# Performance work log

Hardware: AMD Instinct MI355X
Metric: run time of the kernel (lower is better)

## Reference

```python
import jax, jax.numpy as jnp
import numpy as np

B, S, D = 8, 2048, 512

def setup_inputs() -> dict:
    key = jax.random.key(0)
    k1, k2 = jax.random.split(key)
    x = jax.random.normal(k1, (B, S, D), dtype=jnp.float32)
    # nn.Parameter(torch.rand(D, D)) -> uniform [0, 1)
    attn_matrix = jax.random.uniform(k2, (D, D), dtype=jnp.float32)
    return {"x": x, "attn_matrix": attn_matrix}

def reference(x, attn_matrix):
    # scalar = sqrt(last dim of x)
    scale = jnp.sqrt(jnp.asarray(x.shape[-1], dtype=x.dtype))
    # prod = x @ W @ x^T / sqrt(D)  -> [B, S, S]
    xw = jnp.einsum('bsd,de->bse', x, attn_matrix)
    prod = jnp.einsum('bse,bte->bst', xw, x) / scale
    scores = jax.nn.softmax(prod, axis=-1)
    out = jnp.einsum('bst,btd->bsd', scores, x)
    return out
```

## Files before the change

kernel.cpp:

```cpp
#include <hip/hip_runtime.h>
#include <math.h>

#define B_ 8
#define S_ 2048
#define D_ 512
#define HSZ (B_ * S_ * D_)

typedef _Float16 half8 __attribute__((ext_vector_type(8)));
typedef _Float16 half4h __attribute__((ext_vector_type(4)));
typedef __fp16 fp16x2 __attribute__((ext_vector_type(2)));
typedef float f32x4 __attribute__((ext_vector_type(4)));
typedef float f32x16 __attribute__((ext_vector_type(16)));
typedef unsigned int u32;
typedef u32 u32x4 __attribute__((ext_vector_type(4)));

constexpr float INV_SCALE = 0.044194173824159216f;

__device__ __forceinline__ u32 pk16(float a, float b) {
    fp16x2 r = __builtin_amdgcn_cvt_pkrtz(a, b);
    union { fp16x2 h; u32 u; } U; U.h = r; return U.u;
}

__device__ __forceinline__ int offK(int t, int d) {
    return ((t >> 5) << 14) | (((d >> 7) & 3) << 12) | (((d >> 4) & 7) << 9) |
           ((t & 31) << 4) | (((d >> 3) & 1) << 3) | (d & 7);
}
__device__ __forceinline__ int offV(int t, int d) {
    return ((t >> 5) << 14) | (((d >> 7) & 3) << 12) | (((d >> 5) & 3) << 10) |
           (((t >> 4) & 1) << 9) | ((d & 31) << 4) | (((t >> 3) & 1) << 3) | (t & 7);
}
__device__ __forceinline__ int offWT(int n, int k) {
    return ((n >> 5) << 14) | ((k >> 4) << 9) | ((n & 31) << 4) |
           (((k >> 3) & 1) << 3) | (k & 7);
}

__global__ __launch_bounds__(256) void cvt_all(const float* __restrict__ x,
                                               const float* __restrict__ W,
                                               _Float16* __restrict__ xK,
                                               _Float16* __restrict__ xV,
                                               _Float16* __restrict__ WT) {
    __shared__ float T[64 * 65];
    const int tid = threadIdx.x;
    const int blk = blockIdx.x;

    const float* src;
    int t0, d0, isX, bofs = 0;
    if (blk < 2048) {
        int b = blk >> 8;
        int r = blk & 255;
        t0 = (r >> 3) * 64; d0 = (r & 7) * 64;
        src = x + (size_t)b * (S_ * D_);
        bofs = b * (S_ * D_);
        isX = 1;
    } else {
        int r = blk - 2048;
        t0 = (r >> 3) * 64; d0 = (r & 7) * 64;
        src = W;
        isX = 0;
    }

#pragma unroll
    for (int it = 0; it < 4; ++it) {
        int flat = it * 256 + tid;
        int row = flat >> 4, c4 = (flat & 15) * 4;
        float4 v = *(const float4*)(src + (size_t)(t0 + row) * 512 + d0 + c4);
        T[row * 65 + c4 + 0] = v.x; T[row * 65 + c4 + 1] = v.y;
        T[row * 65 + c4 + 2] = v.z; T[row * 65 + c4 + 3] = v.w;
        if (isX) {
            half4h h = { (_Float16)v.x, (_Float16)v.y, (_Float16)v.z, (_Float16)v.w };
            *(half4h*)(xK + bofs + offK(t0 + row, d0 + c4)) = h;
        }
    }
    __syncthreads();
#pragma unroll
    for (int it = 0; it < 2; ++it) {
        int flat = it * 256 + tid;
        int d = flat >> 3, c = (flat & 7) * 8;
        half8 hv;
#pragma unroll
        for (int j = 0; j < 8; ++j) hv[j] = (_Float16)T[(c + j) * 65 + d];
        if (isX)
            *(half8*)(xV + bofs + offV(t0 + c, d0 + d)) = hv;
        else
            *(half8*)(WT + offWT(d0 + d, t0 + c)) = hv;
    }
}

__global__ __launch_bounds__(256, 2) void gemm8(const _Float16* __restrict__ xK,
                                                const _Float16* __restrict__ WT,
                                                _Float16* __restrict__ qwh) {
    const int tid = threadIdx.x;
    const int w = tid >> 6, lane = tid & 63;
    const int r31 = lane & 31, hi = lane >> 5;
    const int laneoff = (r31 << 4) + (hi << 3);
    const int blk = blockIdx.x;
    const int nb = blk & 3;
    const int mb = blk >> 2;
    const int n0w = nb * 128 + w * 32;
    const int batch = mb >> 4;
    const int mt0 = (mb & 15) * 4;
    const size_t bb = (size_t)batch * (S_ * D_);

    half8 Bf[32];
    const _Float16* wb = WT + ((n0w >> 5) << 14) + laneoff;
#pragma unroll
    for (int kc = 0; kc < 32; ++kc) Bf[kc] = *(const half8*)(wb + (kc << 9));

    const _Float16* ab = xK + bb + laneoff;
    const int kk = n0w + r31;
    const int qterm = (((kk >> 7) & 3) << 12) + (((kk >> 4) & 7) << 9) +
                      (((kk >> 3) & 1) << 3) + (kk & 7);

#pragma unroll
    for (int mt = 0; mt < 4; ++mt) {
        const _Float16* at = ab + ((mt0 + mt) << 14);
        f32x16 ca, cb;
#pragma unroll
        for (int r = 0; r < 16; ++r) { ca[r] = 0.f; cb[r] = 0.f; }
#pragma unroll
        for (int kg = 0; kg < 4; ++kg) {
            half8 Af[8];
#pragma unroll
            for (int k8 = 0; k8 < 8; ++k8)
                Af[k8] = *(const half8*)(at + ((kg * 8 + k8) << 9));
#pragma unroll
            for (int k8 = 0; k8 < 8; k8 += 2) {
                ca = __builtin_amdgcn_mfma_f32_32x32x16_f16(Af[k8],     Bf[kg * 8 + k8],     ca, 0, 0, 0);
                cb = __builtin_amdgcn_mfma_f32_32x32x16_f16(Af[k8 + 1], Bf[kg * 8 + k8 + 1], cb, 0, 0, 0);
            }
        }
        _Float16* qp = qwh + bb + ((mt0 + mt) << 14) + qterm;
#pragma unroll
        for (int r = 0; r < 16; ++r) {
            int mrow = (r & 3) + ((r >> 2) << 3) + (hi << 2);
            qp[mrow << 4] = (_Float16)((ca[r] + cb[r]) * INV_SCALE);
        }
    }
}

__global__ __launch_bounds__(256, 2)
void flashP(const _Float16* __restrict__ xK, const _Float16* __restrict__ xV,
            const _Float16* __restrict__ qwh, float* __restrict__ out) {
    __shared__ __align__(16) unsigned char SMEM[34816];
    float* Sx = (float*)SMEM;

    const int tid = threadIdx.x;
    const int w = tid >> 6, lane = tid & 63;
    const int r31 = lane & 31, hi = lane >> 5;
    const int laneoff = (r31 << 4) + (hi << 3);
    const int d0w = w * 128;
    const int bx = blockIdx.x;
    const int b = bx & 7;
    const int q0 = (bx >> 3) * 32;
    const size_t xb = (size_t)b * (S_ * D_);

    half8 Qr[8];
    {
        const _Float16* qb = qwh + xb + ((q0 >> 5) << 14) + (w << 12) + laneoff;
#pragma unroll
        for (int kc = 0; kc < 8; ++kc)
            Qr[kc] = *(const half8*)(qb + (kc << 9));
    }

    const _Float16* kbase = xK + xb + (w << 12) + laneoff;
    const _Float16* vbase = xV + xb + (w << 12) + laneoff;

    half8 KA[8], KB[8];
    f32x16 sS;

#pragma unroll
    for (int kc = 0; kc < 8; ++kc)
        KA[kc] = *(const half8*)(kbase + (kc << 9));
    {
        f32x16 s;
#pragma unroll
        for (int r = 0; r < 16; ++r) s[r] = 0.f;
#pragma unroll
        for (int kc = 0; kc < 8; ++kc)
            s = __builtin_amdgcn_mfma_f32_32x32x16_f16(KA[kc], Qr[kc], s, 0, 0, 0);
        sS = s;
    }
#pragma unroll
    for (int kc = 0; kc < 8; ++kc)
        KB[kc] = *(const half8*)(kbase + (1 << 14) + (kc << 9));
    {
        float* sxw = Sx + w * 1024;
#pragma unroll
        for (int r2 = 0; r2 < 4; ++r2) {
            f32x4 v_ = { sS[4 * r2 + 0], sS[4 * r2 + 1], sS[4 * r2 + 2], sS[4 * r2 + 3] };
            *(f32x4*)&sxw[(r2 * 64 + lane) * 4] = v_;
        }
    }
    __syncthreads();

    f32x16 O[4];
#pragma unroll
    for (int dc = 0; dc < 4; ++dc)
#pragma unroll
        for (int r = 0; r < 16; ++r) O[dc][r] = 0.f;
    float m = -1e30f, l = 0.f;

#define SMX_HEAD(TI) \
    half8 Vc[8]; \
    _Pragma("unroll") for (int dc = 0; dc < 4; ++dc) \
    _Pragma("unroll") for (int kh = 0; kh < 2; ++kh) \
        Vc[dc * 2 + kh] = *(const half8*)(vbase + ((TI) << 14) + (dc << 10) + (kh << 9)); \
    float sv[16]; \
    { \
        _Pragma("unroll") for (int i = 0; i < 16; ++i) sv[i] = sS[i]; \
        _Pragma("unroll") for (int pw = 1; pw < 4; ++pw) { \
            const float* sxp = Sx + (((TI) & 1) * 4 + (w ^ pw)) * 1024; \
            _Pragma("unroll") for (int r2 = 0; r2 < 4; ++r2) { \
                f32x4 pp = *(const f32x4*)&sxp[(r2 * 64 + lane) * 4]; \
                _Pragma("unroll") for (int j = 0; j < 4; ++j) sv[4 * r2 + j] += pp[j]; \
            } \
        } \
    } \
    float mt_ = sv[0]; \
    _Pragma("unroll") for (int i = 1; i < 16; ++i) mt_ = fmaxf(mt_, sv[i]); \
    mt_ = fmaxf(mt_, __shfl_xor(mt_, 32)); \
    if (__any(mt_ > m + 8.f)) { \
        float mn = fmaxf(m, mt_); \
        float a_ = __expf(m - mn); \
        l *= a_; \
        _Pragma("unroll") for (int dc = 0; dc < 4; ++dc) \
        _Pragma("unroll") for (int r = 0; r < 16; ++r) O[dc][r] *= a_; \
        m = mn; \
    } \
    float pa[16]; float rs = 0.f; \
    _Pragma("unroll") for (int i = 0; i < 16; ++i) { pa[i] = __expf(sv[i] - m); rs += pa[i]; } \
    l += rs + __shfl_xor(rs, 32);

#define SMX_TAILPART \
    u32 q16[8]; \
    _Pragma("unroll") for (int r2 = 0; r2 < 4; ++r2) { \
        q16[2 * r2 + 0] = pk16(pa[4 * r2 + 0], pa[4 * r2 + 1]); \
        q16[2 * r2 + 1] = pk16(pa[4 * r2 + 2], pa[4 * r2 + 3]); \
    } \
    half8 Pf[2]; \
    _Pragma("unroll") for (int kh = 0; kh < 2; ++kh) { \
        int r2o = 2 * kh + hi, r2s = 2 * kh + (hi ^ 1); \
        u32 rv0 = (u32)__shfl_xor((int)q16[2 * r2s + 0], 32); \
        u32 rv1 = (u32)__shfl_xor((int)q16[2 * r2s + 1], 32); \
        u32 o0 = q16[2 * r2o + 0], o1 = q16[2 * r2o + 1]; \
        union { u32 u[4]; half8 v; } U_; \
        U_.u[0] = hi ? rv0 : o0; U_.u[1] = hi ? rv1 : o1; \
        U_.u[2] = hi ? o0 : rv0; U_.u[3] = hi ? o1 : rv1; \
        Pf[kh] = U_.v; \
    } \
    _Pragma("unroll") for (int dc = 0; dc < 4; ++dc) { \
        O[dc] = __builtin_amdgcn_mfma_f32_32x32x16_f16(Vc[dc * 2 + 0], Pf[0], O[dc], 0, 0, 0); \
        O[dc] = __builtin_amdgcn_mfma_f32_32x32x16_f16(Vc[dc * 2 + 1], Pf[1], O[dc], 0, 0, 0); \
    }

#define PBODY(TI, KRD, KWR) do {                                                \
    SMX_HEAD(TI)                                                                \
                 \
    f32x16 sn_;                                                                 \
    {                                                                           \
        f32x16 s_;                                                              \
        _Pragma("unroll") for (int r = 0; r < 16; ++r) s_[r] = 0.f;             \
        _Pragma("unroll") for (int kc = 0; kc < 8; ++kc)                        \
            s_ = __builtin_amdgcn_mfma_f32_32x32x16_f16(KRD[kc], Qr[kc], s_, 0, 0, 0); \
        sn_ = s_;                                                               \
    }                                                                           \
                                   \
    {                                                                           \
        const int tp2_ = ((TI) + 2) & 63;                                       \
        _Pragma("unroll") for (int kc = 0; kc < 8; ++kc)                        \
            KWR[kc] = *(const half8*)(kbase + (tp2_ << 14) + (kc << 9));        \
    }                                                                           \
    SMX_TAILPART                                                                \
    sS = sn_;                                                                   \
                                             \
    {                                                                           \
        float* sxw = Sx + ((((TI) + 1) & 1) * 4 + w) * 1024;                    \
        _Pragma("unroll") for (int r2 = 0; r2 < 4; ++r2) {                      \
            f32x4 v_ = { sS[4 * r2 + 0], sS[4 * r2 + 1], sS[4 * r2 + 2], sS[4 * r2 + 3] }; \
            *(f32x4*)&sxw[(r2 * 64 + lane) * 4] = v_;                           \
        }                                                                       \
    }                                                                           \
    __syncthreads();                                                            \
} while (0)

    for (int tp = 0; tp < 31; ++tp) {
        PBODY(2 * tp,     KB, KA);
        PBODY(2 * tp + 1, KA, KB);
    }
    PBODY(62, KB, KA);
    {
        SMX_HEAD(63)
        SMX_TAILPART
    }
#undef PBODY
#undef SMX_HEAD
#undef SMX_TAILPART

    __syncthreads();

    {
        float inv = 1.0f / l;
        float* ew = (float*)SMEM + w * 2176;
        const int qq = lane >> 1, cs = (lane & 1) * 32;
#pragma unroll
        for (int ph = 0; ph < 2; ++ph) {
#pragma unroll
            for (int dc = 0; dc < 2; ++dc)
#pragma unroll
                for (int r = 0; r < 16; ++r) {
                    int dl = dc * 32 + (r & 3) + ((r >> 2) << 3) + (hi << 2);
                    ew[r31 * 68 + dl] = O[ph * 2 + dc][r] * inv;
                }
            float* gp = out + xb + (size_t)(q0 + qq) * 512 + d0w + ph * 64 + cs;
#pragma unroll
            for (int k = 0; k < 8; ++k)
                *(f32x4*)(gp + 4 * k) = *(const f32x4*)&ew[qq * 68 + cs + 4 * k];
        }
    }
}

__global__ __launch_bounds__(256) void xw_gemm_f32(const float* __restrict__ A,
                                                   const float* __restrict__ W,
                                                   float* __restrict__ C) {
    __shared__ float As[16][65];
    __shared__ float Bs[16][64];
    const int tid = threadIdx.x;
    const int row0 = blockIdx.y * 64, col0 = blockIdx.x * 64;
    const int ty = tid / 16, tx = tid % 16;
    float acc[4][4] = {};
    const int ar = tid / 4, ak = (tid % 4) * 4, bk = tid / 16, bn = (tid % 16) * 4;
    for (int k0 = 0; k0 < 512; k0 += 16) {
        float4 a4 = *(const float4*)(A + (size_t)(row0 + ar) * 512 + k0 + ak);
        float4 b4 = *(const float4*)(W + (size_t)(k0 + bk) * 512 + col0 + bn);
        __syncthreads();
        As[ak + 0][ar] = a4.x; As[ak + 1][ar] = a4.y;
        As[ak + 2][ar] = a4.z; As[ak + 3][ar] = a4.w;
        *(float4*)&Bs[bk][bn] = b4;
        __syncthreads();
#pragma unroll
        for (int kk = 0; kk < 16; kk++) {
            float a[4], bv[4];
#pragma unroll
            for (int i = 0; i < 4; i++) a[i] = As[kk][ty * 4 + i];
#pragma unroll
            for (int j = 0; j < 4; j++) bv[j] = Bs[kk][tx * 4 + j];
#pragma unroll
            for (int i = 0; i < 4; i++)
#pragma unroll
                for (int j = 0; j < 4; j++) acc[i][j] += a[i] * bv[j];
        }
    }
#pragma unroll
    for (int i = 0; i < 4; i++) {
        float4 o = make_float4(acc[i][0] * INV_SCALE, acc[i][1] * INV_SCALE,
                               acc[i][2] * INV_SCALE, acc[i][3] * INV_SCALE);
        *(float4*)(C + (size_t)(row0 + ty * 4 + i) * 512 + col0 + tx * 4) = o;
    }
}

__global__ __launch_bounds__(256) void flash_f32(const float* __restrict__ x,
                                                 const float* __restrict__ qw,
                                                 float* __restrict__ out) {
    __shared__ float4 kt[16 * 136];
    const int tid = threadIdx.x;
    const int q = tid >> 3, g = tid & 7;
    const int blk = blockIdx.x;
    const int b = blk >> 6;
    const int qrow = (blk & 63) * 32 + q;
    const size_t xbase = (size_t)b * S_ * D_;
    float qwr[64];
    {
        const float4* p = (const float4*)(qw + xbase + (size_t)qrow * D_ + g * 64);
#pragma unroll
        for (int i4 = 0; i4 < 16; i4++) {
            float4 v = p[i4];
            qwr[4 * i4 + 0] = v.x; qwr[4 * i4 + 1] = v.y;
            qwr[4 * i4 + 2] = v.z; qwr[4 * i4 + 3] = v.w;
        }
    }
    float oa[64];
#pragma unroll
    for (int i = 0; i < 64; i++) oa[i] = 0.f;
    float m = -1e30f, l = 0.f;
    const float4* x4 = (const float4*)(x + xbase);
    for (int t0 = 0; t0 < S_; t0 += 16) {
        __syncthreads();
#pragma unroll
        for (int j = 0; j < 8; j++) {
            int f = tid + j * 256;
            int tt = f >> 7, c = f & 127;
            kt[tt * 136 + (c >> 4) * 17 + (c & 15)] = x4[(size_t)(t0 + tt) * 128 + c];
        }
        __syncthreads();
#pragma unroll 1
        for (int tt = 0; tt < 16; tt++) {
            float4 kv[16];
            const float4* kp = &kt[tt * 136 + g * 17];
#pragma unroll
            for (int i4 = 0; i4 < 16; i4++) kv[i4] = kp[i4];
            float s = 0.f;
#pragma unroll
            for (int i4 = 0; i4 < 16; i4++)
                s += qwr[4 * i4] * kv[i4].x + qwr[4 * i4 + 1] * kv[i4].y
                   + qwr[4 * i4 + 2] * kv[i4].z + qwr[4 * i4 + 3] * kv[i4].w;
            s += __shfl_xor(s, 1, 64); s += __shfl_xor(s, 2, 64); s += __shfl_xor(s, 4, 64);
            if (s > m) {
                float alpha = __expf(m - s);
                l *= alpha;
#pragma unroll
                for (int i = 0; i < 64; i++) oa[i] *= alpha;
                m = s;
            }
            float p = __expf(s - m);
            l += p;
#pragma unroll
            for (int i4 = 0; i4 < 16; i4++) {
                oa[4 * i4 + 0] += p * kv[i4].x; oa[4 * i4 + 1] += p * kv[i4].y;
                oa[4 * i4 + 2] += p * kv[i4].z; oa[4 * i4 + 3] += p * kv[i4].w;
            }
        }
    }
    float inv_l = 1.0f / l;
    float4* op = (float4*)(out + xbase + (size_t)qrow * D_ + g * 64);
#pragma unroll
    for (int i4 = 0; i4 < 16; i4++)
        op[i4] = make_float4(oa[4 * i4] * inv_l, oa[4 * i4 + 1] * inv_l,
                             oa[4 * i4 + 2] * inv_l, oa[4 * i4 + 3] * inv_l);
}

extern "C" void kernel_launch(void* const* d_in, const int* in_sizes, int n_in,
                              void* d_out, int out_size, void* d_ws, size_t ws_size,
                              hipStream_t stream) {
    const float* x = (const float*)d_in[0];
    const float* W = (const float*)d_in[1];
    float* out = (float*)d_out;

    const size_t F16 = (size_t)HSZ * sizeof(_Float16);
    const size_t off_qwh = 0;
    const size_t off_xK  = F16;
    const size_t off_xV  = 2 * F16;
    const size_t off_WT  = 3 * F16;
    const size_t base    = 3 * F16 + 512 * 512 * sizeof(_Float16);

    if (ws_size >= base) {
        _Float16* qwh = (_Float16*)((char*)d_ws + off_qwh);
        _Float16* xK  = (_Float16*)((char*)d_ws + off_xK);
        _Float16* xV  = (_Float16*)((char*)d_ws + off_xV);
        _Float16* WT  = (_Float16*)((char*)d_ws + off_WT);

        cvt_all<<<2112, 256, 0, stream>>>(x, W, xK, xV, WT);
        gemm8<<<512, 256, 0, stream>>>(xK, WT, qwh);
        flashP<<<512, 256, 0, stream>>>(xK, xV, qwh, out);
    } else {
        const size_t needf = (size_t)HSZ * sizeof(float);
        float* xw = (ws_size >= needf) ? (float*)d_ws : out;
        dim3 g1(512 / 64, (B_ * S_) / 64);
        xw_gemm_f32<<<g1, 256, 0, stream>>>(x, W, xw);
        flash_f32<<<B_ * (S_ / 32), 256, 0, stream>>>(x, xw, out);
    }
}
```

Measured before the change: 231.3 us.

## Split flash attention over key range with combine kernel; coalesce gemm8 stores via LDS

```diff
diff --git a/kernel.cpp b/kernel.cpp
--- a/kernel.cpp
+++ b/kernel.cpp
@@ -89,6 +89,7 @@
 __global__ __launch_bounds__(256, 2) void gemm8(const _Float16* __restrict__ xK,
                                                 const _Float16* __restrict__ WT,
                                                 _Float16* __restrict__ qwh) {
+    __shared__ float ldsT[4 * 1152];
     const int tid = threadIdx.x;
     const int w = tid >> 6, lane = tid & 63;
     const int r31 = lane & 31, hi = lane >> 5;
@@ -107,9 +108,8 @@
     for (int kc = 0; kc < 32; ++kc) Bf[kc] = *(const half8*)(wb + (kc << 9));
 
     const _Float16* ab = xK + bb + laneoff;
-    const int kk = n0w + r31;
-    const int qterm = (((kk >> 7) & 3) << 12) + (((kk >> 4) & 7) << 9) +
-                      (((kk >> 3) & 1) << 3) + (kk & 7);
+    float* tw = ldsT + w * 1152;
+    const int mm = lane >> 1, kkg = lane & 1;
 
 #pragma unroll
     for (int mt = 0; mt < 4; ++mt) {
@@ -129,18 +129,30 @@
                 cb = __builtin_amdgcn_mfma_f32_32x32x16_f16(Af[k8 + 1], Bf[kg * 8 + k8 + 1], cb, 0, 0, 0);
             }
         }
-        _Float16* qp = qwh + bb + ((mt0 + mt) << 14) + qterm;
 #pragma unroll
         for (int r = 0; r < 16; ++r) {
             int mrow = (r & 3) + ((r >> 2) << 3) + (hi << 2);
-            qp[mrow << 4] = (_Float16)((ca[r] + cb[r]) * INV_SCALE);
-        }
-    }
-}
-
+            tw[mrow * 36 + r31] = (ca[r] + cb[r]) * INV_SCALE;
+        }
+        _Float16* qb2 = qwh + bb + ((size_t)(mt0 + mt) << 14) + (nb << 12) +
+                        (mm << 4) + (kkg << 3);
+#pragma unroll
+        for (int c8 = 0; c8 < 2; ++c8) {
+            const float* tr = tw + mm * 36 + c8 * 16 + kkg * 8;
+            f32x4 a = *(const f32x4*)(tr);
+            f32x4 bq = *(const f32x4*)(tr + 4);
+            u32x4 st = { pk16(a[0], a[1]), pk16(a[2], a[3]),
+                         pk16(bq[0], bq[1]), pk16(bq[2], bq[3]) };
+            *(u32x4*)(qb2 + ((w * 2 + c8) << 9)) = st;
+        }
+    }
+}
+
+template <int SPLIT>
 __global__ __launch_bounds__(256, 2)
 void flashP(const _Float16* __restrict__ xK, const _Float16* __restrict__ xV,
-            const _Float16* __restrict__ qwh, float* __restrict__ out) {
+            const _Float16* __restrict__ qwh, float* __restrict__ out,
+            _Float16* __restrict__ Os, float* __restrict__ ml) {
     __shared__ __align__(16) unsigned char SMEM[34816];
     float* Sx = (float*)SMEM;
 
@@ -151,7 +163,10 @@
     const int d0w = w * 128;
     const int bx = blockIdx.x;
     const int b = bx & 7;
-    const int q0 = (bx >> 3) * 32;
+    const int q0 = ((bx >> 3) & 63) * 32;
+    const int s = (SPLIT == 2) ? (bx >> 9) : 0;
+    constexpr int NT = 64 / SPLIT;
+    const int soff = s * NT;
     const size_t xb = (size_t)b * (S_ * D_);
 
     half8 Qr[8];
@@ -170,19 +185,19 @@
 
 #pragma unroll
     for (int kc = 0; kc < 8; ++kc)
-        KA[kc] = *(const half8*)(kbase + (kc << 9));
+        KA[kc] = *(const half8*)(kbase + ((size_t)soff << 14) + (kc << 9));
     {
-        f32x16 s;
-#pragma unroll
-        for (int r = 0; r < 16; ++r) s[r] = 0.f;
+        f32x16 sacc;
+#pragma unroll
+        for (int r = 0; r < 16; ++r) sacc[r] = 0.f;
 #pragma unroll
         for (int kc = 0; kc < 8; ++kc)
-            s = __builtin_amdgcn_mfma_f32_32x32x16_f16(KA[kc], Qr[kc], s, 0, 0, 0);
-        sS = s;
+            sacc = __builtin_amdgcn_mfma_f32_32x32x16_f16(KA[kc], Qr[kc], sacc, 0, 0, 0);
+        sS = sacc;
     }
 #pragma unroll
     for (int kc = 0; kc < 8; ++kc)
-        KB[kc] = *(const half8*)(kbase + (1 << 14) + (kc << 9));
+        KB[kc] = *(const half8*)(kbase + ((size_t)(soff + 1) << 14) + (kc << 9));
     {
         float* sxw = Sx + w * 1024;
 #pragma unroll
@@ -204,7 +219,7 @@
     half8 Vc[8]; \
     _Pragma("unroll") for (int dc = 0; dc < 4; ++dc) \
     _Pragma("unroll") for (int kh = 0; kh < 2; ++kh) \
-        Vc[dc * 2 + kh] = *(const half8*)(vbase + ((TI) << 14) + (dc << 10) + (kh << 9)); \
+        Vc[dc * 2 + kh] = *(const half8*)(vbase + ((size_t)(soff + (TI)) << 14) + (dc << 10) + (kh << 9)); \
     float sv[16]; \
     { \
         _Pragma("unroll") for (int i = 0; i < 16; ++i) sv[i] = sS[i]; \
@@ -266,9 +281,9 @@
     }                                                                           \
                                    \
     {                                                                           \
-        const int tp2_ = ((TI) + 2) & 63;                                       \
+        const int tp2_ = soff + (((TI) + 2) & (NT - 1));                        \
         _Pragma("unroll") for (int kc = 0; kc < 8; ++kc)                        \
-            KWR[kc] = *(const half8*)(kbase + (tp2_ << 14) + (kc << 9));        \
+            KWR[kc] = *(const half8*)(kbase + ((size_t)tp2_ << 14) + (kc << 9)); \
     }                                                                           \
     SMX_TAILPART                                                                \
     sS = sn_;                                                                   \
@@ -283,13 +298,13 @@
     __syncthreads();                                                            \
 } while (0)
 
-    for (int tp = 0; tp < 31; ++tp) {
+    for (int tp = 0; tp < NT / 2 - 1; ++tp) {
         PBODY(2 * tp,     KB, KA);
         PBODY(2 * tp + 1, KA, KB);
     }
-    PBODY(62, KB, KA);
+    PBODY(NT - 2, KB, KA);
     {
-        SMX_HEAD(63)
+        SMX_HEAD(NT - 1)
         SMX_TAILPART
     }
 #undef PBODY
@@ -311,11 +326,69 @@
                     int dl = dc * 32 + (r & 3) + ((r >> 2) << 3) + (hi << 2);
                     ew[r31 * 68 + dl] = O[ph * 2 + dc][r] * inv;
                 }
-            float* gp = out + xb + (size_t)(q0 + qq) * 512 + d0w + ph * 64 + cs;
-#pragma unroll
-            for (int k = 0; k < 8; ++k)
-                *(f32x4*)(gp + 4 * k) = *(const f32x4*)&ew[qq * 68 + cs + 4 * k];
-        }
+            if constexpr (SPLIT == 1) {
+                float* gp = out + xb + (size_t)(q0 + qq) * 512 + d0w + ph * 64 + cs;
+#pragma unroll
+                for (int k = 0; k < 8; ++k)
+                    *(f32x4*)(gp + 4 * k) = *(const f32x4*)&ew[qq * 68 + cs + 4 * k];
+            } else {
+                _Float16* op = Os + (size_t)s * HSZ +
+                               ((size_t)b * 2048 + q0 + qq) * 512 + d0w + ph * 64 + cs;
+#pragma unroll
+                for (int g = 0; g < 4; ++g) {
+                    f32x4 va = *(const f32x4*)&ew[qq * 68 + cs + 8 * g];
+                    f32x4 vb = *(const f32x4*)&ew[qq * 68 + cs + 8 * g + 4];
+                    u32x4 st = { pk16(va[0], va[1]), pk16(va[2], va[3]),
+                                 pk16(vb[0], vb[1]), pk16(vb[2], vb[3]) };
+                    *(u32x4*)(op + 8 * g) = st;
+                }
+            }
+        }
+        if constexpr (SPLIT == 2) {
+            if (tid < 32) {
+                int idx = (((s << 3) + b) * 64 + (q0 >> 5)) * 64 + tid * 2;
+                ml[idx] = m; ml[idx + 1] = l;
+            }
+        }
+    }
+}
+
+__global__ __launch_bounds__(256) void combine2(const _Float16* __restrict__ Os,
+                                                const float* __restrict__ ml,
+                                                float* __restrict__ out) {
+    const int tid = threadIdx.x;
+    const int row = blockIdx.x * 8 + (tid >> 5);
+    const int t32 = tid & 31;
+    const int b = row >> 11, q = row & 2047;
+    const int mi = ((b * 64 + (q >> 5)) * 64) + (q & 31) * 2;
+    const float m0 = ml[mi], l0 = ml[mi + 1];
+    const float m1 = ml[(8 * 64 * 64) + mi], l1 = ml[(8 * 64 * 64) + mi + 1];
+    const float mm = fmaxf(m0, m1);
+    const float a0 = l0 * __expf(m0 - mm), a1 = l1 * __expf(m1 - mm);
+    const float inv = 1.0f / (a0 + a1);
+    const float w0 = a0 * inv, w1 = a1 * inv;
+
+    const size_t e = (size_t)row * 512 + t32 * 16;
+    half8 p0a = *(const half8*)(Os + e);
+    half8 p0b = *(const half8*)(Os + e + 8);
+    half8 p1a = *(const half8*)(Os + (size_t)HSZ + e);
+    half8 p1b = *(const half8*)(Os + (size_t)HSZ + e + 8);
+    float* gp = out + e;
+#pragma unroll
+    for (int g = 0; g < 2; ++g) {
+        f32x4 o;
+#pragma unroll
+        for (int j = 0; j < 4; ++j)
+            o[j] = w0 * (float)p0a[g * 4 + j] + w1 * (float)p1a[g * 4 + j];
+        *(f32x4*)(gp + g * 4) = o;
+    }
+#pragma unroll
+    for (int g = 0; g < 2; ++g) {
+        f32x4 o;
+#pragma unroll
+        for (int j = 0; j < 4; ++j)
+            o[j] = w0 * (float)p0b[g * 4 + j] + w1 * (float)p1b[g * 4 + j];
+        *(f32x4*)(gp + 8 + g * 4) = o;
     }
 }
 
@@ -441,6 +514,9 @@
     const size_t off_xV  = 2 * F16;
     const size_t off_WT  = 3 * F16;
     const size_t base    = 3 * F16 + 512 * 512 * sizeof(_Float16);
+    const size_t off_Os  = base;
+    const size_t off_ml  = base + 2 * F16;
+    const size_t need2   = base + 2 * F16 + (size_t)(2 * 8 * 64 * 64) * sizeof(float);
 
     if (ws_size >= base) {
         _Float16* qwh = (_Float16*)((char*)d_ws + off_qwh);
@@ -450,7 +526,14 @@
 
         cvt_all<<<2112, 256, 0, stream>>>(x, W, xK, xV, WT);
         gemm8<<<512, 256, 0, stream>>>(xK, WT, qwh);
-        flashP<<<512, 256, 0, stream>>>(xK, xV, qwh, out);
+        if (ws_size >= need2) {
+            _Float16* Os = (_Float16*)((char*)d_ws + off_Os);
+            float* ml    = (float*)((char*)d_ws + off_ml);
+            flashP<2><<<1024, 256, 0, stream>>>(xK, xV, qwh, out, Os, ml);
+            combine2<<<2048, 256, 0, stream>>>(Os, ml, out);
+        } else {
+            flashP<1><<<512, 256, 0, stream>>>(xK, xV, qwh, out, nullptr, nullptr);
+        }
     } else {
         const size_t needf = (size_t)HSZ * sizeof(float);
         float* xw = (ws_size >= needf) ? (float*)d_ws : out;
```

New measurement: 250.8 us. 1.08x slower.

## Fuse x fp16 conversion and layout packing into the xW GEMM kernel

Applied to the files above, without the earlier changes.

```diff
diff --git a/kernel.cpp b/kernel.cpp
--- a/kernel.cpp
+++ b/kernel.cpp
@@ -21,55 +21,20 @@
     union { fp16x2 h; u32 u; } U; U.h = r; return U.u;
 }
 
-__device__ __forceinline__ int offK(int t, int d) {
-    return ((t >> 5) << 14) | (((d >> 7) & 3) << 12) | (((d >> 4) & 7) << 9) |
-           ((t & 31) << 4) | (((d >> 3) & 1) << 3) | (d & 7);
-}
-__device__ __forceinline__ int offV(int t, int d) {
-    return ((t >> 5) << 14) | (((d >> 7) & 3) << 12) | (((d >> 5) & 3) << 10) |
-           (((t >> 4) & 1) << 9) | ((d & 31) << 4) | (((t >> 3) & 1) << 3) | (t & 7);
-}
-__device__ __forceinline__ int offWT(int n, int k) {
-    return ((n >> 5) << 14) | ((k >> 4) << 9) | ((n & 31) << 4) |
-           (((k >> 3) & 1) << 3) | (k & 7);
-}
-
-__global__ __launch_bounds__(256) void cvt_all(const float* __restrict__ x,
-                                               const float* __restrict__ W,
-                                               _Float16* __restrict__ xK,
-                                               _Float16* __restrict__ xV,
-                                               _Float16* __restrict__ WT) {
+__global__ __launch_bounds__(256) void cvtW(const float* __restrict__ W,
+                                            _Float16* __restrict__ WT) {
     __shared__ float T[64 * 65];
     const int tid = threadIdx.x;
-    const int blk = blockIdx.x;
-
-    const float* src;
-    int t0, d0, isX, bofs = 0;
-    if (blk < 2048) {
-        int b = blk >> 8;
-        int r = blk & 255;
-        t0 = (r >> 3) * 64; d0 = (r & 7) * 64;
-        src = x + (size_t)b * (S_ * D_);
-        bofs = b * (S_ * D_);
-        isX = 1;
-    } else {
-        int r = blk - 2048;
-        t0 = (r >> 3) * 64; d0 = (r & 7) * 64;
-        src = W;
-        isX = 0;
-    }
+    const int r = blockIdx.x;
+    const int t0 = (r >> 3) * 64, d0 = (r & 7) * 64;
 
 #pragma unroll
     for (int it = 0; it < 4; ++it) {
         int flat = it * 256 + tid;
         int row = flat >> 4, c4 = (flat & 15) * 4;
-        float4 v = *(const float4*)(src + (size_t)(t0 + row) * 512 + d0 + c4);
+        float4 v = *(const float4*)(W + (size_t)(t0 + row) * 512 + d0 + c4);
         T[row * 65 + c4 + 0] = v.x; T[row * 65 + c4 + 1] = v.y;
         T[row * 65 + c4 + 2] = v.z; T[row * 65 + c4 + 3] = v.w;
-        if (isX) {
-            half4h h = { (_Float16)v.x, (_Float16)v.y, (_Float16)v.z, (_Float16)v.w };
-            *(half4h*)(xK + bofs + offK(t0 + row, d0 + c4)) = h;
-        }
     }
     __syncthreads();
 #pragma unroll
@@ -79,61 +44,113 @@
         half8 hv;
 #pragma unroll
         for (int j = 0; j < 8; ++j) hv[j] = (_Float16)T[(c + j) * 65 + d];
-        if (isX)
-            *(half8*)(xV + bofs + offV(t0 + c, d0 + d)) = hv;
-        else
-            *(half8*)(WT + offWT(d0 + d, t0 + c)) = hv;
-    }
-}
-
-__global__ __launch_bounds__(256, 2) void gemm8(const _Float16* __restrict__ xK,
-                                                const _Float16* __restrict__ WT,
-                                                _Float16* __restrict__ qwh) {
+        int n = d0 + d, k = t0 + c;
+        int off = ((n >> 5) << 14) | ((k >> 4) << 9) | ((n & 31) << 4) |
+                  (((k >> 3) & 1) << 3) | (k & 7);
+        *(half8*)(WT + off) = hv;
+    }
+}
+
+__global__ __launch_bounds__(256, 2)
+void gemmF(const float* __restrict__ x, const _Float16* __restrict__ WT,
+           _Float16* __restrict__ xK, _Float16* __restrict__ xV,
+           _Float16* __restrict__ qwh) {
+    __shared__ float T[32 * 516];
     const int tid = threadIdx.x;
     const int w = tid >> 6, lane = tid & 63;
     const int r31 = lane & 31, hi = lane >> 5;
     const int laneoff = (r31 << 4) + (hi << 3);
     const int blk = blockIdx.x;
-    const int nb = blk & 3;
-    const int mb = blk >> 2;
-    const int n0w = nb * 128 + w * 32;
-    const int batch = mb >> 4;
-    const int mt0 = (mb & 15) * 4;
-    const size_t bb = (size_t)batch * (S_ * D_);
-
-    half8 Bf[32];
-    const _Float16* wb = WT + ((n0w >> 5) << 14) + laneoff;
-#pragma unroll
-    for (int kc = 0; kc < 32; ++kc) Bf[kc] = *(const half8*)(wb + (kc << 9));
-
-    const _Float16* ab = xK + bb + laneoff;
-    const int kk = n0w + r31;
-    const int qterm = (((kk >> 7) & 3) << 12) + (((kk >> 4) & 7) << 9) +
-                      (((kk >> 3) & 1) << 3) + (kk & 7);
-
-#pragma unroll
-    for (int mt = 0; mt < 4; ++mt) {
-        const _Float16* at = ab + ((mt0 + mt) << 14);
-        f32x16 ca, cb;
-#pragma unroll
-        for (int r = 0; r < 16; ++r) { ca[r] = 0.f; cb[r] = 0.f; }
-#pragma unroll
-        for (int kg = 0; kg < 4; ++kg) {
-            half8 Af[8];
-#pragma unroll
-            for (int k8 = 0; k8 < 8; ++k8)
-                Af[k8] = *(const half8*)(at + ((kg * 8 + k8) << 9));
-#pragma unroll
-            for (int k8 = 0; k8 < 8; k8 += 2) {
-                ca = __builtin_amdgcn_mfma_f32_32x32x16_f16(Af[k8],     Bf[kg * 8 + k8],     ca, 0, 0, 0);
-                cb = __builtin_amdgcn_mfma_f32_32x32x16_f16(Af[k8 + 1], Bf[kg * 8 + k8 + 1], cb, 0, 0, 0);
+    const int b = blk & 7;
+    const int mt = blk >> 3;
+    const size_t bb = (size_t)b * (S_ * D_);
+
+    {
+        const float* xs = x + bb + (size_t)(mt * 32) * 512;
+#pragma unroll
+        for (int it = 0; it < 16; ++it) {
+            int f = it * 256 + tid;
+            int row = f >> 7, c4 = (f & 127) << 2;
+            float4 v = *(const float4*)(xs + (size_t)row * 512 + c4);
+            *(float4*)&T[row * 516 + c4] = v;
+        }
+    }
+    __syncthreads();
+
+    {
+        _Float16* xvb = xV + bb + ((size_t)mt << 14) + (w << 12);
+#pragma unroll
+        for (int dc = 0; dc < 4; ++dc)
+#pragma unroll
+            for (int kh = 0; kh < 2; ++kh) {
+                int d = w * 128 + dc * 32 + r31;
+                half8 v;
+#pragma unroll
+                for (int j = 0; j < 8; ++j)
+                    v[j] = (_Float16)T[(kh * 16 + hi * 8 + j) * 516 + d];
+                *(half8*)(xvb + (dc << 10) + (kh << 9) + laneoff) = v;
             }
-        }
-        _Float16* qp = qwh + bb + ((mt0 + mt) << 14) + qterm;
-#pragma unroll
-        for (int r = 0; r < 16; ++r) {
-            int mrow = (r & 3) + ((r >> 2) << 3) + (hi << 2);
-            qp[mrow << 4] = (_Float16)((ca[r] + cb[r]) * INV_SCALE);
+    }
+
+    f32x16 acc[4];
+#pragma unroll
+    for (int nt = 0; nt < 4; ++nt)
+#pragma unroll
+        for (int r = 0; r < 16; ++r) acc[nt][r] = 0.f;
+
+    const _Float16* wtb = WT + ((w * 4) << 14) + laneoff;
+    _Float16* xkb = xK + bb + ((size_t)mt << 14);
+
+    for (int ph = 0; ph < 2; ++ph) {
+        half8 A[16];
+#pragma unroll
+        for (int kc8 = 0; kc8 < 16; ++kc8) {
+            int kc = ph * 16 + kc8;
+            const float* tr = &T[r31 * 516 + kc * 16 + hi * 8];
+            half8 a;
+#pragma unroll
+            for (int j = 0; j < 8; ++j) a[j] = (_Float16)tr[j];
+            A[kc8] = a;
+            if ((kc & 3) == w)
+                *(half8*)(xkb + (kc << 9) + laneoff) = a;
+        }
+#pragma unroll
+        for (int kc8 = 0; kc8 < 16; ++kc8) {
+            int kc = ph * 16 + kc8;
+            half8 B0 = *(const half8*)(wtb + (0 << 14) + (kc << 9));
+            half8 B1 = *(const half8*)(wtb + (1 << 14) + (kc << 9));
+            half8 B2 = *(const half8*)(wtb + (2 << 14) + (kc << 9));
+            half8 B3 = *(const half8*)(wtb + (3 << 14) + (kc << 9));
+            acc[0] = __builtin_amdgcn_mfma_f32_32x32x16_f16(A[kc8], B0, acc[0], 0, 0, 0);
+            acc[1] = __builtin_amdgcn_mfma_f32_32x32x16_f16(A[kc8], B1, acc[1], 0, 0, 0);
+            acc[2] = __builtin_amdgcn_mfma_f32_32x32x16_f16(A[kc8], B2, acc[2], 0, 0, 0);
+            acc[3] = __builtin_amdgcn_mfma_f32_32x32x16_f16(A[kc8], B3, acc[3], 0, 0, 0);
+        }
+    }
+
+    __syncthreads();
+
+    {
+        float* tw = T + w * 1152;
+        const int mm = lane >> 1, kkg = lane & 1;
+        _Float16* qb2 = qwh + bb + ((size_t)mt << 14) + (w << 12) +
+                        (mm << 4) + (kkg << 3);
+#pragma unroll
+        for (int nt = 0; nt < 4; ++nt) {
+#pragma unroll
+            for (int r = 0; r < 16; ++r) {
+                int mrow = (r & 3) + ((r >> 2) << 3) + (hi << 2);
+                tw[mrow * 36 + r31] = acc[nt][r] * INV_SCALE;
+            }
+#pragma unroll
+            for (int c8 = 0; c8 < 2; ++c8) {
+                const float* tr2 = tw + mm * 36 + c8 * 16 + kkg * 8;
+                f32x4 a = *(const f32x4*)(tr2);
+                f32x4 bq = *(const f32x4*)(tr2 + 4);
+                u32x4 st = { pk16(a[0], a[1]), pk16(a[2], a[3]),
+                             pk16(bq[0], bq[1]), pk16(bq[2], bq[3]) };
+                *(u32x4*)(qb2 + ((nt * 2 + c8) << 9)) = st;
+            }
         }
     }
 }
@@ -272,7 +289,6 @@
     }                                                                           \
     SMX_TAILPART                                                                \
     sS = sn_;                                                                   \
-                                             \
     {                                                                           \
         float* sxw = Sx + ((((TI) + 1) & 1) * 4 + w) * 1024;                    \
         _Pragma("unroll") for (int r2 = 0; r2 < 4; ++r2) {                      \
@@ -448,8 +464,8 @@
         _Float16* xV  = (_Float16*)((char*)d_ws + off_xV);
         _Float16* WT  = (_Float16*)((char*)d_ws + off_WT);
 
-        cvt_all<<<2112, 256, 0, stream>>>(x, W, xK, xV, WT);
-        gemm8<<<512, 256, 0, stream>>>(xK, WT, qwh);
+        cvtW<<<64, 256, 0, stream>>>(W, WT);
+        gemmF<<<512, 256, 0, stream>>>(x, WT, xK, xV, qwh);
         flashP<<<512, 256, 0, stream>>>(xK, xV, qwh, out);
     } else {
         const size_t needf = (size_t)HSZ * sizeof(float);
```

After: 227.4 us. About the same (-1.7%).

## Fuse x@W projection into flash attention kernel prologue, drop separate GEMM

Applied to the files above, without the earlier changes.

```diff
diff --git a/kernel.cpp b/kernel.cpp
--- a/kernel.cpp
+++ b/kernel.cpp
@@ -86,61 +86,9 @@
     }
 }
 
-__global__ __launch_bounds__(256, 2) void gemm8(const _Float16* __restrict__ xK,
-                                                const _Float16* __restrict__ WT,
-                                                _Float16* __restrict__ qwh) {
-    const int tid = threadIdx.x;
-    const int w = tid >> 6, lane = tid & 63;
-    const int r31 = lane & 31, hi = lane >> 5;
-    const int laneoff = (r31 << 4) + (hi << 3);
-    const int blk = blockIdx.x;
-    const int nb = blk & 3;
-    const int mb = blk >> 2;
-    const int n0w = nb * 128 + w * 32;
-    const int batch = mb >> 4;
-    const int mt0 = (mb & 15) * 4;
-    const size_t bb = (size_t)batch * (S_ * D_);
-
-    half8 Bf[32];
-    const _Float16* wb = WT + ((n0w >> 5) << 14) + laneoff;
-#pragma unroll
-    for (int kc = 0; kc < 32; ++kc) Bf[kc] = *(const half8*)(wb + (kc << 9));
-
-    const _Float16* ab = xK + bb + laneoff;
-    const int kk = n0w + r31;
-    const int qterm = (((kk >> 7) & 3) << 12) + (((kk >> 4) & 7) << 9) +
-                      (((kk >> 3) & 1) << 3) + (kk & 7);
-
-#pragma unroll
-    for (int mt = 0; mt < 4; ++mt) {
-        const _Float16* at = ab + ((mt0 + mt) << 14);
-        f32x16 ca, cb;
-#pragma unroll
-        for (int r = 0; r < 16; ++r) { ca[r] = 0.f; cb[r] = 0.f; }
-#pragma unroll
-        for (int kg = 0; kg < 4; ++kg) {
-            half8 Af[8];
-#pragma unroll
-            for (int k8 = 0; k8 < 8; ++k8)
-                Af[k8] = *(const half8*)(at + ((kg * 8 + k8) << 9));
-#pragma unroll
-            for (int k8 = 0; k8 < 8; k8 += 2) {
-                ca = __builtin_amdgcn_mfma_f32_32x32x16_f16(Af[k8],     Bf[kg * 8 + k8],     ca, 0, 0, 0);
-                cb = __builtin_amdgcn_mfma_f32_32x32x16_f16(Af[k8 + 1], Bf[kg * 8 + k8 + 1], cb, 0, 0, 0);
-            }
-        }
-        _Float16* qp = qwh + bb + ((mt0 + mt) << 14) + qterm;
-#pragma unroll
-        for (int r = 0; r < 16; ++r) {
-            int mrow = (r & 3) + ((r >> 2) << 3) + (hi << 2);
-            qp[mrow << 4] = (_Float16)((ca[r] + cb[r]) * INV_SCALE);
-        }
-    }
-}
-
 __global__ __launch_bounds__(256, 2)
-void flashP(const _Float16* __restrict__ xK, const _Float16* __restrict__ xV,
-            const _Float16* __restrict__ qwh, float* __restrict__ out) {
+void flashF(const _Float16* __restrict__ xK, const _Float16* __restrict__ xV,
+            const _Float16* __restrict__ WT, float* __restrict__ out) {
     __shared__ __align__(16) unsigned char SMEM[34816];
     float* Sx = (float*)SMEM;
 
@@ -154,16 +102,58 @@
     const int q0 = (bx >> 3) * 32;
     const size_t xb = (size_t)b * (S_ * D_);
 
-    half8 Qr[8];
-    {
-        const _Float16* qb = qwh + xb + ((q0 >> 5) << 14) + (w << 12) + laneoff;
-#pragma unroll
-        for (int kc = 0; kc < 8; ++kc)
-            Qr[kc] = *(const half8*)(qb + (kc << 9));
-    }
-
     const _Float16* kbase = xK + xb + (w << 12) + laneoff;
     const _Float16* vbase = xV + xb + (w << 12) + laneoff;
+
+    half8 Qr[8];
+    {
+        const _Float16* aq = xK + xb + ((size_t)(q0 >> 5) << 14) + laneoff;
+        const _Float16* wtb = WT + ((w * 4) << 14) + laneoff;
+        f32x16 acc[4];
+#pragma unroll
+        for (int nt = 0; nt < 4; ++nt)
+#pragma unroll
+            for (int r = 0; r < 16; ++r) acc[nt][r] = 0.f;
+#pragma unroll
+        for (int kg = 0; kg < 4; ++kg) {
+            half8 Ax[8];
+#pragma unroll
+            for (int k8 = 0; k8 < 8; ++k8)
+                Ax[k8] = *(const half8*)(aq + ((kg * 8 + k8) << 9));
+#pragma unroll
+            for (int k8 = 0; k8 < 8; ++k8) {
+                int kc = kg * 8 + k8;
+                half8 B0 = *(const half8*)(wtb + (0 << 14) + (kc << 9));
+                half8 B1 = *(const half8*)(wtb + (1 << 14) + (kc << 9));
+                half8 B2 = *(const half8*)(wtb + (2 << 14) + (kc << 9));
+                half8 B3 = *(const half8*)(wtb + (3 << 14) + (kc << 9));
+                acc[0] = __builtin_amdgcn_mfma_f32_32x32x16_f16(Ax[k8], B0, acc[0], 0, 0, 0);
+                acc[1] = __builtin_amdgcn_mfma_f32_32x32x16_f16(Ax[k8], B1, acc[1], 0, 0, 0);
+                acc[2] = __builtin_amdgcn_mfma_f32_32x32x16_f16(Ax[k8], B2, acc[2], 0, 0, 0);
+                acc[3] = __builtin_amdgcn_mfma_f32_32x32x16_f16(Ax[k8], B3, acc[3], 0, 0, 0);
+            }
+        }
+        float* tw = (float*)SMEM + w * 1152;
+#pragma unroll
+        for (int nt = 0; nt < 4; ++nt) {
+#pragma unroll
+            for (int r = 0; r < 16; ++r) {
+                int mrow = (r & 3) + ((r >> 2) << 3) + (hi << 2);
+                tw[mrow * 36 + r31] = acc[nt][r] * INV_SCALE;
+            }
+#pragma unroll
+            for (int h2 = 0; h2 < 2; ++h2) {
+                const float* tr = tw + r31 * 36 + h2 * 16 + hi * 8;
+                f32x4 a = *(const f32x4*)(tr);
+                f32x4 b4 = *(const f32x4*)(tr + 4);
+                half8 q;
+#pragma unroll
+                for (int j = 0; j < 4; ++j) { q[j] = (_Float16)a[j]; q[4 + j] = (_Float16)b4[j]; }
+                Qr[2 * nt + h2] = q;
+            }
+        }
+    }
+    __syncthreads();
 
     half8 KA[8], KB[8];
     f32x16 sS;
@@ -255,7 +245,6 @@
 
 #define PBODY(TI, KRD, KWR) do {                                                \
     SMX_HEAD(TI)                                                                \
-                 \
     f32x16 sn_;                                                                 \
     {                                                                           \
         f32x16 s_;                                                              \
@@ -264,7 +253,6 @@
             s_ = __builtin_amdgcn_mfma_f32_32x32x16_f16(KRD[kc], Qr[kc], s_, 0, 0, 0); \
         sn_ = s_;                                                               \
     }                                                                           \
-                                   \
     {                                                                           \
         const int tp2_ = ((TI) + 2) & 63;                                       \
         _Pragma("unroll") for (int kc = 0; kc < 8; ++kc)                        \
@@ -272,7 +260,6 @@
     }                                                                           \
     SMX_TAILPART                                                                \
     sS = sn_;                                                                   \
-                                             \
     {                                                                           \
         float* sxw = Sx + ((((TI) + 1) & 1) * 4 + w) * 1024;                    \
         _Pragma("unroll") for (int r2 = 0; r2 < 4; ++r2) {                      \
@@ -436,21 +423,18 @@
     float* out = (float*)d_out;
 
     const size_t F16 = (size_t)HSZ * sizeof(_Float16);
-    const size_t off_qwh = 0;
-    const size_t off_xK  = F16;
-    const size_t off_xV  = 2 * F16;
-    const size_t off_WT  = 3 * F16;
-    const size_t base    = 3 * F16 + 512 * 512 * sizeof(_Float16);
+    const size_t off_xK = 0;
+    const size_t off_xV = F16;
+    const size_t off_WT = 2 * F16;
+    const size_t base   = 2 * F16 + 512 * 512 * sizeof(_Float16);
 
     if (ws_size >= base) {
-        _Float16* qwh = (_Float16*)((char*)d_ws + off_qwh);
-        _Float16* xK  = (_Float16*)((char*)d_ws + off_xK);
-        _Float16* xV  = (_Float16*)((char*)d_ws + off_xV);
-        _Float16* WT  = (_Float16*)((char*)d_ws + off_WT);
+        _Float16* xK = (_Float16*)((char*)d_ws + off_xK);
+        _Float16* xV = (_Float16*)((char*)d_ws + off_xV);
+        _Float16* WT = (_Float16*)((char*)d_ws + off_WT);
 
         cvt_all<<<2112, 256, 0, stream>>>(x, W, xK, xV, WT);
-        gemm8<<<512, 256, 0, stream>>>(xK, WT, qwh);
-        flashP<<<512, 256, 0, stream>>>(xK, xV, qwh, out);
+        flashF<<<512, 256, 0, stream>>>(xK, xV, WT, out);
     } else {
         const size_t needf = (size_t)HSZ * sizeof(float);
         float* xw = (ws_size >= needf) ? (float*)d_ws : out;
```

Measured after the change: 222.9 us. 3.6% less time.
